# Performance work log

Measured on AMD Instinct MI355X. Metric: run time of the kernel, lower is better.

Reference implementation:

```python
import jax, jax.numpy as jnp
import numpy as np

HEADS = 8
DIM_HEAD = 64
SCALE = DIM_HEAD ** -0.5


def setup_inputs() -> dict:
    key = jax.random.key(0)
    k1, k2, k3 = jax.random.split(key, 3)
    b, n, dim = 2, 4096, 512
    inner = HEADS * DIM_HEAD  # 512
    x = jax.random.normal(k1, (b, n, dim), dtype=jnp.float32)
    # torch Linear weight is [out, in]; store transposed [in, out] for x @ W
    w_qkv = jax.random.normal(k2, (dim, inner), dtype=jnp.float32) * (dim ** -0.5)
    w_out = jax.random.normal(k3, (inner, dim), dtype=jnp.float32) * (inner ** -0.5)
    b_out = jnp.zeros((dim,), dtype=jnp.float32)
    return {"x": x, "w_qkv": w_qkv, "w_out": w_out, "b_out": b_out}


def reference(x, w_qkv, w_out, b_out):
    b, n, _ = x.shape
    # shared projection: w acts as q = k = v
    w = (x @ w_qkv).reshape(b, n, HEADS, DIM_HEAD).transpose(0, 2, 1, 3)  # b h n d
    dots = jnp.einsum('bhid,bhjd->bhij', w, w) * SCALE                    # b h n n
    attn = jax.nn.softmax(dots, axis=-1)
    out = jnp.einsum('bhij,bhjd->bhid', attn, w)                          # b h n d
    out = out.transpose(0, 2, 1, 3).reshape(b, n, HEADS * DIM_HEAD)       # b n (h d)
    return out @ w_out + b_out
```

## Files before the change

kernel.cpp:

```cpp
#include <hip/hip_runtime.h>

typedef __attribute__((ext_vector_type(8))) short short8;
typedef __attribute__((ext_vector_type(8))) unsigned short u16x8;
typedef __attribute__((ext_vector_type(4))) float f32x4;
typedef __attribute__((ext_vector_type(16))) float f32x16;
typedef __attribute__((ext_vector_type(4))) unsigned int u32x4;

#define MFMA16 __builtin_amdgcn_mfma_f32_16x16x32_bf16
#define MFMA32 __builtin_amdgcn_mfma_f32_32x32x16_bf16

__device__ __forceinline__ unsigned short f2bf(float f) {
  unsigned int u = __builtin_bit_cast(unsigned int, f);
  u = (u + 0x7FFFu + ((u >> 16) & 1u)) >> 16;
  return (unsigned short)u;
}

__device__ __forceinline__ unsigned int cvt_pk_bf16(float lo, float hi) {
  unsigned int r;
  asm("v_cvt_pk_bf16_f32 %0, %1, %2" : "=v"(r) : "v"(lo), "v"(hi));
  return r;
}

__device__ __forceinline__ void pl32_swap(unsigned int& a, unsigned int& b) {
  asm("v_permlane32_swap_b32 %0, %1" : "+v"(a), "+v"(b));
}

__device__ __forceinline__ float exp2_raw(float x) {
  float r;
  asm("v_exp_f32 %0, %1" : "=v"(r) : "v"(x));
  return r;
}

#define GLOAD_LDS16(g, l)                                                   \
  __builtin_amdgcn_global_load_lds(                                         \
      (const __attribute__((address_space(1))) unsigned int*)(g),           \
      (__attribute__((address_space(3))) unsigned int*)(l), 16, 0, 0)

#define ALPHA 0.42466089f

__global__ __launch_bounds__(256) void san_prep(const float* __restrict__ x,
                                                const float* __restrict__ wqkv,
                                                unsigned short* __restrict__ xf,
                                                unsigned short* __restrict__ qkf) {
  const int bid = blockIdx.x, t = threadIdx.x;
  if (bid < 2048) {
    int cid = bid * 256 + t;
    int l = cid & 63, msub = (cid >> 6) & 7, kt = (cid >> 9) & 15, mt = cid >> 13;
    int row = mt * 128 + msub * 16 + (l & 15);
    int col = kt * 32 + (l >> 4) * 8;
    const float* src = x + (size_t)row * 512 + col;
    f32x4 v0 = *(const f32x4*)(src);
    f32x4 v1 = *(const f32x4*)(src + 4);
    unsigned short tmp[8];
    #pragma unroll
    for (int e = 0; e < 4; ++e) { tmp[e] = f2bf(v0[e]); tmp[4 + e] = f2bf(v1[e]); }
    *(u16x8*)(xf + (size_t)cid * 8) = *(u16x8*)tmp;
  } else {
    int c = (bid - 2048) * 256 + t;
    int l = c & 63, nsub = (c >> 6) & 3, kt = (c >> 8) & 15, nt = c >> 12;
    int n = nt * 64 + nsub * 16 + (l & 15);
    int k0 = kt * 32 + (l >> 4) * 8;
    unsigned short tmp[8];
    #pragma unroll
    for (int e = 0; e < 8; ++e) tmp[e] = f2bf(wqkv[(size_t)(k0 + e) * 512 + n]);
    *(u16x8*)(qkf + (size_t)c * 8) = *(u16x8*)tmp;
  }
}

__global__ __launch_bounds__(256) void san_qkv(const unsigned short* __restrict__ xf,
                                               const unsigned short* __restrict__ qkf,
                                               unsigned short* __restrict__ wf,
                                               unsigned short* __restrict__ vtf) {
  __shared__ char smem[24576];
  const int t = threadIdx.x;
  const int mt = blockIdx.x >> 3, nt = blockIdx.x & 7;
  const int m0 = mt * 128, n0 = nt * 64;
  const int lane = t & 63, wv = t >> 6;
  const int wr = wv >> 1, wc = wv & 1;
  const int lr = lane & 15, lg = lane >> 4;

  f32x4 acc[4][2];
  #pragma unroll
  for (int m = 0; m < 4; ++m)
    #pragma unroll
    for (int n = 0; n < 2; ++n) acc[m][n] = (f32x4){0.f, 0.f, 0.f, 0.f};

  auto stage = [&](int buf, int kt) {
    const char* asrc = (const char*)xf + (((size_t)mt * 16 + kt) << 13);
    GLOAD_LDS16(asrc + t * 16, smem + buf * 8192 + t * 16);
    GLOAD_LDS16(asrc + 4096 + t * 16, smem + buf * 8192 + 4096 + t * 16);
    const char* bsrc = (const char*)qkf + (((size_t)nt * 16 + kt) << 12);
    GLOAD_LDS16(bsrc + t * 16, smem + 16384 + buf * 4096 + t * 16);
  };
  auto compute = [&](int buf) {
    const char* ab = smem + buf * 8192;
    const char* bb = smem + 16384 + buf * 4096;
    short8 af[4], bfr[2];
    #pragma unroll
    for (int m = 0; m < 4; ++m)
      af[m] = *(const short8*)(ab + (wr * 4 + m) * 1024 + lane * 16);
    #pragma unroll
    for (int n = 0; n < 2; ++n)
      bfr[n] = *(const short8*)(bb + (wc * 2 + n) * 1024 + lane * 16);
    #pragma unroll
    for (int m = 0; m < 4; ++m)
      #pragma unroll
      for (int n = 0; n < 2; ++n)
        acc[m][n] = MFMA16(af[m], bfr[n], acc[m][n], 0, 0, 0);
  };

  stage(0, 0);
  __syncthreads();
  for (int kt = 0; kt < 16; ++kt) {
    if (kt + 1 < 16) stage((kt + 1) & 1, kt + 1);
    compute(kt & 1);
    __syncthreads();
  }

  #pragma unroll
  for (int m = 0; m < 4; ++m)
    #pragma unroll
    for (int n = 0; n < 2; ++n) {
      int gcol = n0 + wc * 32 + n * 16 + lr;
      int h = gcol >> 6, d = gcol & 63;
      int grow0 = m0 + wr * 64 + m * 16 + lg * 4;
      int b = grow0 >> 12, nn0 = grow0 & 4095;
      size_t hb = (size_t)((b << 3) + h);
      size_t tbase = (hb << 18) + ((size_t)(nn0 >> 6) << 12);
      int sd = d >> 4, hid = (d >> 3) & 1, e = d & 7;
      #pragma unroll
      for (int r = 0; r < 4; ++r) {
        int nn = nn0 + r;
        int jh = (nn >> 5) & 1;
        int l  = (nn & 31) | (hid << 5);
        wf[tbase + (size_t)((((jh << 2) + sd) << 9) + (l << 3) + e)] =
            f2bf(acc[m][n][r] * ALPHA);
      }
      unsigned int p0 = cvt_pk_bf16(acc[m][n][0], acc[m][n][1]);
      unsigned int p1 = cvt_pk_bf16(acc[m][n][2], acc[m][n][3]);
      int dh = d >> 5, sj = (nn0 >> 4) & 3;
      int lv = (d & 31) | (((nn0 >> 3) & 1) << 5);
      unsigned short* vp =
          vtf + tbase + (size_t)((((dh << 2) + sj) << 9) + (lv << 3) + (nn0 & 7));
      *(unsigned int*)(vp)     = p0;
      *(unsigned int*)(vp + 2) = p1;
    }
}

__global__ __launch_bounds__(512, 4) void san_attn(
    const unsigned short* __restrict__ wf, const unsigned short* __restrict__ vtf,
    unsigned short* __restrict__ of) {
  __shared__ char smem[65536];
  const int t = threadIdx.x;
  const int lane = t & 63, wp = t >> 6;
  const int lo5 = lane & 31, hi = lane >> 5;
  const int qg = wp & 3, kvhalf = wp >> 2;
  const int bid = blockIdx.x;
  const int bh = ((bid & 7) << 1) + ((bid >> 3) & 1);
  const int qblk = bid >> 4;
  const unsigned short* whf = wf + ((size_t)bh << 18);
  const unsigned short* wthf = vtf + ((size_t)bh << 18);

  const int qrow = qblk * 128 + qg * 32 + lo5;
  const int jtq = qrow >> 6, jhq = (qrow >> 5) & 1;
  const unsigned short* qb = whf + ((size_t)jtq << 12) + ((jhq << 2) << 9) +
                             (((qrow & 31) | (hi << 5)) << 3);
  short8 qf0 = *(const short8*)(qb + 0 * 512);
  short8 qf1 = *(const short8*)(qb + 1 * 512);
  short8 qf2 = *(const short8*)(qb + 2 * 512);
  short8 qf3 = *(const short8*)(qb + 3 * 512);

  f32x16 oacc0, oacc1, fz;
  #pragma unroll
  for (int r = 0; r < 16; ++r) { oacc0[r] = 0.f; oacc1[r] = 0.f; fz[r] = 0.f; }
  float l_run = 0.f;

  auto stage = [&](int buf, int jt) {
    #pragma unroll
    for (int h = 0; h < 2; ++h) {
      int gt = h * 32 + jt;
      const char* ksrc = (const char*)whf + ((size_t)gt << 13) + t * 16;
      GLOAD_LDS16(ksrc, smem + (buf * 2 + h) * 8192 + t * 16);
      const char* vsrc = (const char*)wthf + ((size_t)gt << 13) + t * 16;
      GLOAD_LDS16(vsrc, smem + 32768 + (buf * 2 + h) * 8192 + t * 16);
    }
  };

  auto computeTile = [&](const char* kb, const char* vb) {
    f32x16 st0, st1;
    __builtin_amdgcn_s_setprio(1);
    {
      short8 k0v = *(const short8*)(kb + 0 * 1024 + lane * 16);
      short8 k1v = *(const short8*)(kb + 1 * 1024 + lane * 16);
      short8 k2v = *(const short8*)(kb + 2 * 1024 + lane * 16);
      short8 k3v = *(const short8*)(kb + 3 * 1024 + lane * 16);
      st0 = MFMA32(k0v, qf0, fz, 0, 0, 0);
      st0 = MFMA32(k1v, qf1, st0, 0, 0, 0);
      st0 = MFMA32(k2v, qf2, st0, 0, 0, 0);
      st0 = MFMA32(k3v, qf3, st0, 0, 0, 0);
    }
    {
      short8 k0v = *(const short8*)(kb + 4096 + 0 * 1024 + lane * 16);
      short8 k1v = *(const short8*)(kb + 4096 + 1 * 1024 + lane * 16);
      short8 k2v = *(const short8*)(kb + 4096 + 2 * 1024 + lane * 16);
      short8 k3v = *(const short8*)(kb + 4096 + 3 * 1024 + lane * 16);
      st1 = MFMA32(k0v, qf0, fz, 0, 0, 0);
      st1 = MFMA32(k1v, qf1, st1, 0, 0, 0);
      st1 = MFMA32(k2v, qf2, st1, 0, 0, 0);
      st1 = MFMA32(k3v, qf3, st1, 0, 0, 0);
    }
    __builtin_amdgcn_s_setprio(0);

    float ps0 = 0.f, ps1 = 0.f, ps2 = 0.f, ps3 = 0.f;
    #pragma unroll
    for (int r = 0; r < 16; ++r) {
      float p = exp2_raw(st0[r]);
      st0[r] = p;
      if ((r & 3) == 0) ps0 += p; else if ((r & 3) == 1) ps1 += p;
      else if ((r & 3) == 2) ps2 += p; else ps3 += p;
    }
    #pragma unroll
    for (int r = 0; r < 16; ++r) {
      float p = exp2_raw(st1[r]);
      st1[r] = p;
      if ((r & 3) == 0) ps0 += p; else if ((r & 3) == 1) ps1 += p;
      else if ((r & 3) == 2) ps2 += p; else ps3 += p;
    }
    l_run += (ps0 + ps1) + (ps2 + ps3);

    unsigned int c0 = cvt_pk_bf16(st0[0], st0[1]);
    unsigned int c1 = cvt_pk_bf16(st0[2], st0[3]);
    unsigned int c2 = cvt_pk_bf16(st0[4], st0[5]);
    unsigned int c3 = cvt_pk_bf16(st0[6], st0[7]);
    unsigned int c4 = cvt_pk_bf16(st0[8], st0[9]);
    unsigned int c5 = cvt_pk_bf16(st0[10], st0[11]);
    unsigned int c6 = cvt_pk_bf16(st0[12], st0[13]);
    unsigned int c7 = cvt_pk_bf16(st0[14], st0[15]);
    pl32_swap(c0, c2); pl32_swap(c1, c3);
    pl32_swap(c4, c6); pl32_swap(c5, c7);
    u32x4 u0 = {c0, c1, c2, c3}, u1 = {c4, c5, c6, c7};
    short8 pf0 = __builtin_bit_cast(short8, u0);
    short8 pf1 = __builtin_bit_cast(short8, u1);
    c0 = cvt_pk_bf16(st1[0], st1[1]);
    c1 = cvt_pk_bf16(st1[2], st1[3]);
    c2 = cvt_pk_bf16(st1[4], st1[5]);
    c3 = cvt_pk_bf16(st1[6], st1[7]);
    c4 = cvt_pk_bf16(st1[8], st1[9]);
    c5 = cvt_pk_bf16(st1[10], st1[11]);
    c6 = cvt_pk_bf16(st1[12], st1[13]);
    c7 = cvt_pk_bf16(st1[14], st1[15]);
    pl32_swap(c0, c2); pl32_swap(c1, c3);
    pl32_swap(c4, c6); pl32_swap(c5, c7);
    u32x4 u2 = {c0, c1, c2, c3}, u3 = {c4, c5, c6, c7};
    short8 pf2 = __builtin_bit_cast(short8, u2);
    short8 pf3 = __builtin_bit_cast(short8, u3);

    __builtin_amdgcn_s_setprio(1);
    #pragma unroll
    for (int s = 0; s < 4; ++s) {
      short8 vfr = *(const short8*)(vb + s * 1024 + lane * 16);
      oacc0 = MFMA32(vfr, (s == 0 ? pf0 : s == 1 ? pf1 : s == 2 ? pf2 : pf3), oacc0, 0, 0, 0);
    }
    #pragma unroll
    for (int s = 0; s < 4; ++s) {
      short8 vfr = *(const short8*)(vb + 4096 + s * 1024 + lane * 16);
      oacc1 = MFMA32(vfr, (s == 0 ? pf0 : s == 1 ? pf1 : s == 2 ? pf2 : pf3), oacc1, 0, 0, 0);
    }
    __builtin_amdgcn_s_setprio(0);
  };

  auto kbuf = [&](int buf) { return (const char*)(smem + (buf * 2 + kvhalf) * 8192); };
  auto vbuf = [&](int buf) { return (const char*)(smem + 32768 + (buf * 2 + kvhalf) * 8192); };

  stage(0, 0);
  __syncthreads();
  for (int jt = 0; jt < 32; jt += 2) {
    stage(1, jt + 1);
    computeTile(kbuf(0), vbuf(0));
    __syncthreads();
    if (jt + 2 < 32) stage(0, jt + 2);
    computeTile(kbuf(1), vbuf(1));
    __syncthreads();
  }

  float l_tot = l_run + __shfl_xor(l_run, 32);

  float* scratch = (float*)smem;
  float* obase = scratch + qg * 2112;
  if (kvhalf == 1) {
    #pragma unroll
    for (int c = 0; c < 4; ++c) {
      f32x4 v = {oacc0[4 * c], oacc0[4 * c + 1], oacc0[4 * c + 2], oacc0[4 * c + 3]};
      *(f32x4*)(obase + c * 256 + lane * 4) = v;
    }
    #pragma unroll
    for (int c = 0; c < 4; ++c) {
      f32x4 v = {oacc1[4 * c], oacc1[4 * c + 1], oacc1[4 * c + 2], oacc1[4 * c + 3]};
      *(f32x4*)(obase + 1024 + c * 256 + lane * 4) = v;
    }
    obase[2048 + lane] = l_tot;
  }
  __syncthreads();
  if (kvhalf == 0) {
    float l_b = obase[2048 + lane];
    float linv = 1.f / (l_tot + l_b);
    float ob0[16], ob1[16];
    #pragma unroll
    for (int c = 0; c < 4; ++c) {
      f32x4 v = *(const f32x4*)(obase + c * 256 + lane * 4);
      #pragma unroll
      for (int e = 0; e < 4; ++e) ob0[4 * c + e] = v[e];
    }
    #pragma unroll
    for (int c = 0; c < 4; ++c) {
      f32x4 v = *(const f32x4*)(obase + 1024 + c * 256 + lane * 4);
      #pragma unroll
      for (int e = 0; e < 4; ++e) ob1[4 * c + e] = v[e];
    }
    const int token = ((bh >> 3) << 12) + qrow;
    const int h = bh & 7;
    const int mt = token >> 7, msub = (token >> 4) & 7;
    char* ofb = (char*)of;
    #pragma unroll
    for (int i = 0; i < 8; ++i) {
      float a0 = (oacc0[2 * i] + ob0[2 * i]) * linv;
      float a1 = (oacc0[2 * i + 1] + ob0[2 * i + 1]) * linv;
      float b0 = (oacc1[2 * i] + ob1[2 * i]) * linv;
      float b1 = (oacc1[2 * i + 1] + ob1[2 * i + 1]) * linv;
      unsigned int pk0 = cvt_pk_bf16(a0, a1);
      unsigned int pk1 = cvt_pk_bf16(b0, b1);
      int dl = ((2 * i) & 3) + 8 * ((2 * i) >> 2) + 4 * hi;
      size_t addr = (((size_t)mt * 16 + h * 2) << 13) + msub * 1024 +
                    (((token & 15) | ((dl >> 3) << 4)) << 4) + (dl & 7) * 2;
      *(unsigned int*)(ofb + addr) = pk0;
      *(unsigned int*)(ofb + addr + 8192) = pk1;
    }
  }
}

__global__ __launch_bounds__(256) void san_out(const unsigned short* __restrict__ of,
                                               const float* __restrict__ wo,
                                               const float* __restrict__ bias,
                                               float* __restrict__ out) {
  __shared__ char Asm[16384];
  __shared__ unsigned short Blds[2][64 * 40];
  const int t = threadIdx.x;
  const int mt = blockIdx.x >> 3;
  const int m0 = mt * 128, n0 = (blockIdx.x & 7) * 64;
  const int lane = t & 63, wv = t >> 6;
  const int wr = wv >> 1, wc = wv & 1;
  const int lr = lane & 15, lg = lane >> 4;

  f32x4 acc[4][2];
  #pragma unroll
  for (int m = 0; m < 4; ++m)
    #pragma unroll
    for (int n = 0; n < 2; ++n) acc[m][n] = (f32x4){0.f, 0.f, 0.f, 0.f};

  auto stageA = [&](int buf, int kt) {
    const char* asrc = (const char*)of + (((size_t)mt * 16 + kt) << 13);
    GLOAD_LDS16(asrc + t * 16, Asm + buf * 8192 + t * 16);
    GLOAD_LDS16(asrc + 4096 + t * 16, Asm + buf * 8192 + 4096 + t * 16);
  };
  auto convB = [&](int buf, int kt) {
    const int k = t & 31, nb = (t >> 5) * 8;
    const float* src = wo + (size_t)(kt * 32 + k) * 512 + n0 + nb;
    #pragma unroll
    for (int i = 0; i < 8; i += 4) {
      f32x4 v = *(const f32x4*)(src + i);
      #pragma unroll
      for (int e = 0; e < 4; ++e) Blds[buf][(nb + i + e) * 40 + k] = f2bf(v[e]);
    }
  };
  auto compute = [&](int buf) {
    const char* ab = Asm + buf * 8192;
    short8 af[4], bfr[2];
    #pragma unroll
    for (int m = 0; m < 4; ++m)
      af[m] = *(const short8*)(ab + (wr * 4 + m) * 1024 + lane * 16);
    #pragma unroll
    for (int n = 0; n < 2; ++n)
      bfr[n] = *(const short8*)&Blds[buf][(wc * 32 + n * 16 + lr) * 40 + lg * 8];
    #pragma unroll
    for (int m = 0; m < 4; ++m)
      #pragma unroll
      for (int n = 0; n < 2; ++n)
        acc[m][n] = MFMA16(af[m], bfr[n], acc[m][n], 0, 0, 0);
  };

  stageA(0, 0); convB(0, 0);
  __syncthreads();
  for (int kt = 0; kt < 16; ++kt) {
    if (kt + 1 < 16) { stageA((kt + 1) & 1, kt + 1); convB((kt + 1) & 1, kt + 1); }
    compute(kt & 1);
    __syncthreads();
  }

  #pragma unroll
  for (int m = 0; m < 4; ++m)
    #pragma unroll
    for (int n = 0; n < 2; ++n)
      #pragma unroll
      for (int r = 0; r < 4; ++r) {
        int grow = m0 + wr * 64 + m * 16 + lg * 4 + r;
        int gcol = n0 + wc * 32 + n * 16 + lr;
        out[(size_t)grow * 512 + gcol] = acc[m][n][r] + bias[gcol];
      }
}

extern "C" void kernel_launch(void* const* d_in, const int* in_sizes, int n_in,
                              void* d_out, int out_size, void* d_ws, size_t ws_size,
                              hipStream_t stream) {
  const float* x    = (const float*)d_in[0];
  const float* wqkv = (const float*)d_in[1];
  const float* wo   = (const float*)d_in[2];
  const float* bias = (const float*)d_in[3];
  float* out = (float*)d_out;

  unsigned short* wff = (unsigned short*)d_ws;
  unsigned short* off = wff + (size_t)2 * 8 * 4096 * 64;
  unsigned short* vtf = off + (size_t)2 * 8 * 4096 * 64;
  unsigned short* xf  = (unsigned short*)d_out;
  unsigned short* qkf = xf + (size_t)4 * 1024 * 1024;

  san_prep<<<dim3(2176), dim3(256), 0, stream>>>(x, wqkv, xf, qkf);
  san_qkv<<<dim3(512), dim3(256), 0, stream>>>(xf, qkf, wff, vtf);
  san_attn<<<dim3(512), dim3(512), 0, stream>>>(wff, vtf, off);
  san_out<<<dim3(512), dim3(256), 0, stream>>>(off, wo, bias, out);
}
```

Before: 117.2 us.

## Pre-convert output weights to bf16 fragments and vectorize softmax row-sum accumulation

The prep kernel now also converts w_out to bf16 in MFMA fragment order when the workspace is large enough. The output GEMM can then stage B tiles with direct global-to-LDS loads instead of converting fp32 to bf16 in every block. In the attention kernel, the exp row sums are accumulated as packed float2 vectors instead of four scalar partial sums. This adds 128 prep blocks and a workspace-size dependent path, and falls back to the old conversion when the workspace is too small.

```diff
diff --git a/kernel.cpp b/kernel.cpp
--- a/kernel.cpp
+++ b/kernel.cpp
@@ -2,6 +2,7 @@
 
 typedef __attribute__((ext_vector_type(8))) short short8;
 typedef __attribute__((ext_vector_type(8))) unsigned short u16x8;
+typedef __attribute__((ext_vector_type(2))) float f32x2;
 typedef __attribute__((ext_vector_type(4))) float f32x4;
 typedef __attribute__((ext_vector_type(16))) float f32x16;
 typedef __attribute__((ext_vector_type(4))) unsigned int u32x4;
@@ -40,8 +41,10 @@
 
 __global__ __launch_bounds__(256) void san_prep(const float* __restrict__ x,
                                                 const float* __restrict__ wqkv,
+                                                const float* __restrict__ wo,
                                                 unsigned short* __restrict__ xf,
-                                                unsigned short* __restrict__ qkf) {
+                                                unsigned short* __restrict__ qkf,
+                                                unsigned short* __restrict__ wof) {
   const int bid = blockIdx.x, t = threadIdx.x;
   if (bid < 2048) {
     int cid = bid * 256 + t;
@@ -55,7 +58,7 @@
     #pragma unroll
     for (int e = 0; e < 4; ++e) { tmp[e] = f2bf(v0[e]); tmp[4 + e] = f2bf(v1[e]); }
     *(u16x8*)(xf + (size_t)cid * 8) = *(u16x8*)tmp;
-  } else {
+  } else if (bid < 2176) {
     int c = (bid - 2048) * 256 + t;
     int l = c & 63, nsub = (c >> 6) & 3, kt = (c >> 8) & 15, nt = c >> 12;
     int n = nt * 64 + nsub * 16 + (l & 15);
@@ -64,6 +67,15 @@
     #pragma unroll
     for (int e = 0; e < 8; ++e) tmp[e] = f2bf(wqkv[(size_t)(k0 + e) * 512 + n]);
     *(u16x8*)(qkf + (size_t)c * 8) = *(u16x8*)tmp;
+  } else {
+    int c = (bid - 2176) * 256 + t;
+    int l = c & 63, nsub = (c >> 6) & 3, kt = (c >> 8) & 15, nt = c >> 12;
+    int n = nt * 64 + nsub * 16 + (l & 15);
+    int k0 = kt * 32 + (l >> 4) * 8;
+    unsigned short tmp[8];
+    #pragma unroll
+    for (int e = 0; e < 8; ++e) tmp[e] = f2bf(wo[(size_t)(k0 + e) * 512 + n]);
+    *(u16x8*)(wof + (size_t)c * 8) = *(u16x8*)tmp;
   }
 }
 
@@ -173,7 +185,7 @@
   f32x16 oacc0, oacc1, fz;
   #pragma unroll
   for (int r = 0; r < 16; ++r) { oacc0[r] = 0.f; oacc1[r] = 0.f; fz[r] = 0.f; }
-  float l_run = 0.f;
+  f32x2 lacc01 = {0.f, 0.f}, lacc23 = {0.f, 0.f};
 
   auto stage = [&](int buf, int jt) {
     #pragma unroll
@@ -211,22 +223,22 @@
     }
     __builtin_amdgcn_s_setprio(0);
 
-    float ps0 = 0.f, ps1 = 0.f, ps2 = 0.f, ps3 = 0.f;
-    #pragma unroll
-    for (int r = 0; r < 16; ++r) {
-      float p = exp2_raw(st0[r]);
-      st0[r] = p;
-      if ((r & 3) == 0) ps0 += p; else if ((r & 3) == 1) ps1 += p;
-      else if ((r & 3) == 2) ps2 += p; else ps3 += p;
-    }
-    #pragma unroll
-    for (int r = 0; r < 16; ++r) {
-      float p = exp2_raw(st1[r]);
-      st1[r] = p;
-      if ((r & 3) == 0) ps0 += p; else if ((r & 3) == 1) ps1 += p;
-      else if ((r & 3) == 2) ps2 += p; else ps3 += p;
-    }
-    l_run += (ps0 + ps1) + (ps2 + ps3);
+    #pragma unroll
+    for (int r = 0; r < 8; ++r) {
+      float p0 = exp2_raw(st0[2 * r]);
+      float p1 = exp2_raw(st0[2 * r + 1]);
+      st0[2 * r] = p0; st0[2 * r + 1] = p1;
+      f32x2 pv = {p0, p1};
+      if (r & 1) lacc23 += pv; else lacc01 += pv;
+    }
+    #pragma unroll
+    for (int r = 0; r < 8; ++r) {
+      float p0 = exp2_raw(st1[2 * r]);
+      float p1 = exp2_raw(st1[2 * r + 1]);
+      st1[2 * r] = p0; st1[2 * r + 1] = p1;
+      f32x2 pv = {p0, p1};
+      if (r & 1) lacc23 += pv; else lacc01 += pv;
+    }
 
     unsigned int c0 = cvt_pk_bf16(st0[0], st0[1]);
     unsigned int c1 = cvt_pk_bf16(st0[2], st0[3]);
@@ -283,6 +295,8 @@
     __syncthreads();
   }
 
+  f32x2 lp = lacc01 + lacc23;
+  float l_run = lp[0] + lp[1];
   float l_tot = l_run + __shfl_xor(l_run, 32);
 
   float* scratch = (float*)smem;
@@ -339,17 +353,19 @@
 }
 
 __global__ __launch_bounds__(256) void san_out(const unsigned short* __restrict__ of,
+                                               const unsigned short* __restrict__ wof,
                                                const float* __restrict__ wo,
                                                const float* __restrict__ bias,
                                                float* __restrict__ out) {
   __shared__ char Asm[16384];
-  __shared__ unsigned short Blds[2][64 * 40];
+  __shared__ char Bsm[2][5120];
   const int t = threadIdx.x;
-  const int mt = blockIdx.x >> 3;
-  const int m0 = mt * 128, n0 = (blockIdx.x & 7) * 64;
+  const int mt = blockIdx.x >> 3, nt = blockIdx.x & 7;
+  const int m0 = mt * 128, n0 = nt * 64;
   const int lane = t & 63, wv = t >> 6;
   const int wr = wv >> 1, wc = wv & 1;
   const int lr = lane & 15, lg = lane >> 4;
+  const bool frag = (wof != nullptr);
 
   f32x4 acc[4][2];
   #pragma unroll
@@ -362,14 +378,20 @@
     GLOAD_LDS16(asrc + t * 16, Asm + buf * 8192 + t * 16);
     GLOAD_LDS16(asrc + 4096 + t * 16, Asm + buf * 8192 + 4096 + t * 16);
   };
-  auto convB = [&](int buf, int kt) {
-    const int k = t & 31, nb = (t >> 5) * 8;
-    const float* src = wo + (size_t)(kt * 32 + k) * 512 + n0 + nb;
-    #pragma unroll
-    for (int i = 0; i < 8; i += 4) {
-      f32x4 v = *(const f32x4*)(src + i);
-      #pragma unroll
-      for (int e = 0; e < 4; ++e) Blds[buf][(nb + i + e) * 40 + k] = f2bf(v[e]);
+  auto stageB = [&](int buf, int kt) {
+    if (frag) {
+      const char* bsrc = (const char*)wof + (((size_t)nt * 16 + kt) << 12);
+      GLOAD_LDS16(bsrc + t * 16, Bsm[buf] + t * 16);
+    } else {
+      const int k = t & 31, nb = (t >> 5) * 8;
+      const float* src = wo + (size_t)(kt * 32 + k) * 512 + n0 + nb;
+      unsigned short* bl = (unsigned short*)Bsm[buf];
+      #pragma unroll
+      for (int i = 0; i < 8; i += 4) {
+        f32x4 v = *(const f32x4*)(src + i);
+        #pragma unroll
+        for (int e = 0; e < 4; ++e) bl[(nb + i + e) * 40 + k] = f2bf(v[e]);
+      }
     }
   };
   auto compute = [&](int buf) {
@@ -378,9 +400,16 @@
     #pragma unroll
     for (int m = 0; m < 4; ++m)
       af[m] = *(const short8*)(ab + (wr * 4 + m) * 1024 + lane * 16);
-    #pragma unroll
-    for (int n = 0; n < 2; ++n)
-      bfr[n] = *(const short8*)&Blds[buf][(wc * 32 + n * 16 + lr) * 40 + lg * 8];
+    if (frag) {
+      #pragma unroll
+      for (int n = 0; n < 2; ++n)
+        bfr[n] = *(const short8*)(Bsm[buf] + (wc * 2 + n) * 1024 + lane * 16);
+    } else {
+      const unsigned short* bl = (const unsigned short*)Bsm[buf];
+      #pragma unroll
+      for (int n = 0; n < 2; ++n)
+        bfr[n] = *(const short8*)&bl[(wc * 32 + n * 16 + lr) * 40 + lg * 8];
+    }
     #pragma unroll
     for (int m = 0; m < 4; ++m)
       #pragma unroll
@@ -388,10 +417,10 @@
         acc[m][n] = MFMA16(af[m], bfr[n], acc[m][n], 0, 0, 0);
   };
 
-  stageA(0, 0); convB(0, 0);
+  stageA(0, 0); stageB(0, 0);
   __syncthreads();
   for (int kt = 0; kt < 16; ++kt) {
-    if (kt + 1 < 16) { stageA((kt + 1) & 1, kt + 1); convB((kt + 1) & 1, kt + 1); }
+    if (kt + 1 < 16) { stageA((kt + 1) & 1, kt + 1); stageB((kt + 1) & 1, kt + 1); }
     compute(kt & 1);
     __syncthreads();
   }
@@ -423,8 +452,12 @@
   unsigned short* xf  = (unsigned short*)d_out;
   unsigned short* qkf = xf + (size_t)4 * 1024 * 1024;
 
-  san_prep<<<dim3(2176), dim3(256), 0, stream>>>(x, wqkv, xf, qkf);
+  const bool big_ws = ws_size >= (size_t)25 * 1024 * 1024;
+  unsigned short* wof = big_ws ? (vtf + (size_t)2 * 8 * 4096 * 64) : nullptr;
+
+  san_prep<<<dim3(big_ws ? 2304 : 2176), dim3(256), 0, stream>>>(
+      x, wqkv, wo, xf, qkf, wof);
   san_qkv<<<dim3(512), dim3(256), 0, stream>>>(xf, qkf, wff, vtf);
   san_attn<<<dim3(512), dim3(512), 0, stream>>>(wff, vtf, off);
-  san_out<<<dim3(512), dim3(256), 0, stream>>>(off, wo, bias, out);
-}
+  san_out<<<dim3(512), dim3(256), 0, stream>>>(off, wof, wo, bias, out);
+}
```

New measurement: 116.1 us. About the same (-0.9%).
